# Performance work log

Measured on AMD Instinct MI355X. Metric: run time of the kernel, lower is better.

## Reference

```python
import jax, jax.numpy as jnp
import numpy as np

N = 1024   # num nodes
D = 128    # feat_dim (input_dim)


def setup_inputs() -> dict:
    key = jax.random.key(0)
    k1, k2 = jax.random.split(key)
    x = jax.random.normal(k1, (N, D), dtype=jnp.float32)
    # nn.Linear(D, 1) -> weight vector [D], bias [1] (xavier init weight, zero bias)
    w_vec = jax.random.normal(k2, (D,), dtype=jnp.float32) * np.sqrt(2.0 / (D + 1))
    w_bias = jnp.zeros((1,), dtype=jnp.float32)
    return {"x": x, "w_vec": w_vec, "w_bias": w_bias}


def reference(x, w_vec, w_bias):
    # diff[i, j, d] = |x[i, d] - x[j, d]|  (repeat_interleave row-major -> x[i] minus broadcast x[j])
    diff = jnp.abs(x[:, None, :] - x[None, :, :])          # [N, N, D]
    scores = jnp.einsum('ijd,d->ij', diff, w_vec) + w_bias[0]  # Linear(D,1) -> [N, N]
    scores = jax.nn.relu(scores)
    return jax.nn.softmax(scores, axis=1)
```

## Files before the change

### kernel.cpp

```cpp
#include <hip/hip_runtime.h>

#define N 1024
#define D 128
#define PAD 132

__global__ __launch_bounds__(512, 4) void scores_kernel(
    const float* __restrict__ x, const float* __restrict__ w,
    const float* __restrict__ bias, float* __restrict__ E,
    float* __restrict__ part) {
  __shared__ float sxi[64 * PAD];
  __shared__ float sxj[32 * PAD];
  __shared__ float sw[D];

  const int t  = threadIdx.x;
  const int bi = blockIdx.y * 64;
  const int bj = blockIdx.x * 32;

  {
    const int c  = t & 31;
    const int r0 = t >> 5;
    #pragma unroll
    for (int p = 0; p < 4; ++p) {
      const int r = r0 + p * 16;
      const float4 v = reinterpret_cast<const float4*>(x)[(bi + r) * 32 + c];
      *reinterpret_cast<float4*>(&sxi[r * PAD + c * 4]) = v;
    }
    #pragma unroll
    for (int p = 0; p < 2; ++p) {
      const int r = r0 + p * 16;
      const float4 v = reinterpret_cast<const float4*>(x)[(bj + r) * 32 + c];
      *reinterpret_cast<float4*>(&sxj[r * PAD + c * 4]) = v;
    }
    if (t < 32)
      *reinterpret_cast<float4*>(&sw[t * 4]) =
          reinterpret_cast<const float4*>(w)[t];
  }
  __syncthreads();

  const int g  = __builtin_amdgcn_readfirstlane(t >> 8);
  const int s  = t & 255;
  const int tx = s & 15;
  const int ty = s >> 4;
  const int d0 = g * 64;

  float acc[4][2];
  #pragma unroll
  for (int a = 0; a < 4; ++a)
    #pragma unroll
    for (int b = 0; b < 2; ++b) acc[a][b] = 0.f;

  #pragma unroll 4
  for (int dc = 0; dc < 16; ++dc) {
    const int d = d0 + dc * 4;
    const float4 W = *reinterpret_cast<const float4*>(&sw[d]);
    float4 A[4], B[2];
    #pragma unroll
    for (int a = 0; a < 4; ++a)
      A[a] = *reinterpret_cast<const float4*>(&sxi[(ty + 16 * a) * PAD + d]);
    #pragma unroll
    for (int b = 0; b < 2; ++b)
      B[b] = *reinterpret_cast<const float4*>(&sxj[(tx + 16 * b) * PAD + d]);

    #pragma unroll
    for (int a = 0; a < 4; ++a) {
      #pragma unroll
      for (int b = 0; b < 2; ++b) {
        float v = acc[a][b];
        v = fmaf(fabsf(A[a].x - B[b].x), W.x, v);
        v = fmaf(fabsf(A[a].y - B[b].y), W.y, v);
        v = fmaf(fabsf(A[a].z - B[b].z), W.z, v);
        v = fmaf(fabsf(A[a].w - B[b].w), W.w, v);
        acc[a][b] = v;
      }
    }
  }
  __syncthreads();

  float* comb = sxi;
  if (g == 1) {
    float* dst = comb + s * 9;
    #pragma unroll
    for (int k = 0; k < 8; ++k) dst[k] = acc[k >> 1][k & 1];
  }
  __syncthreads();

  if (g == 0) {
    const float* src = comb + s * 9;
    #pragma unroll
    for (int k = 0; k < 8; ++k) acc[k >> 1][k & 1] += src[k];

    const float bv = bias[0];
    #pragma unroll
    for (int a = 0; a < 4; ++a) {
      float p = 0.f;
      #pragma unroll
      for (int b = 0; b < 2; ++b) {
        const float ev = __expf(fmaxf(acc[a][b] + bv, 0.f));
        acc[a][b] = ev;
        p += ev;
      }
      #pragma unroll
      for (int o = 1; o < 16; o <<= 1) p += __shfl_xor(p, o, 64);
      if (tx == 0) part[(bi + ty + 16 * a) * 32 + blockIdx.x] = p;
    }

    #pragma unroll
    for (int a = 0; a < 4; ++a) {
      const int row = bi + ty + 16 * a;
      #pragma unroll
      for (int b = 0; b < 2; ++b)
        E[row * N + bj + tx + 16 * b] = acc[a][b];
    }
  }
}

__global__ __launch_bounds__(256) void scale_kernel(
    float* __restrict__ S, const float* __restrict__ part) {
  const int row = blockIdx.x;
  const int t   = threadIdx.x;

  float p = part[row * 32 + (t & 31)];
  #pragma unroll
  for (int o = 1; o < 32; o <<= 1) p += __shfl_xor(p, o, 64);
  const float r = 1.0f / p;

  float4* rowp = reinterpret_cast<float4*>(S + row * N);
  float4 v = rowp[t];
  v.x *= r; v.y *= r; v.z *= r; v.w *= r;
  rowp[t] = v;
}

extern "C" void kernel_launch(void* const* d_in, const int* in_sizes, int n_in,
                              void* d_out, int out_size, void* d_ws, size_t ws_size,
                              hipStream_t stream) {
  const float* x = (const float*)d_in[0];
  const float* w = (const float*)d_in[1];
  const float* b = (const float*)d_in[2];
  float* out  = (float*)d_out;
  float* part = (float*)d_ws;

  dim3 grid(N / 32, N / 64);
  scores_kernel<<<grid, 512, 0, stream>>>(x, w, b, out, part);
  scale_kernel<<<N, 256, 0, stream>>>(out, part);
}
```

Measured before the change: 72.83 us.

## Exploit score matrix symmetry by computing only upper-triangle tiles

The pairwise score matrix is symmetric, so the kernel now computes only tiles with block-row index p <= block-column q, decoding each triangle tile index with a sqrt plus correction loop. For off-diagonal tiles it transposes the exponentiated values through shared memory and writes the mirrored tile, emitting separate row-sum partials for the direct and mirrored parts. The scale kernel combines both partial arrays per row. Block size shrinks to 128 threads with a 16x32 tile and the split-D reduction is removed. This roughly halves the abs-diff FMA work at the cost of extra transposed stores, a shared-memory sync and more, smaller blocks.

```diff
diff --git a/kernel.cpp b/kernel.cpp
--- a/kernel.cpp
+++ b/kernel.cpp
@@ -4,32 +4,40 @@
 #define D 128
 #define PAD 132
 
-__global__ __launch_bounds__(512, 4) void scores_kernel(
+__global__ __launch_bounds__(128, 2) void scores_kernel(
     const float* __restrict__ x, const float* __restrict__ w,
     const float* __restrict__ bias, float* __restrict__ E,
-    float* __restrict__ part) {
-  __shared__ float sxi[64 * PAD];
+    float* __restrict__ partA, float* __restrict__ partB) {
+  __shared__ float sxi[16 * PAD];
   __shared__ float sxj[32 * PAD];
   __shared__ float sw[D];
+  __shared__ float ldst[16 * 33];
 
-  const int t  = threadIdx.x;
-  const int bi = blockIdx.y * 64;
-  const int bj = blockIdx.x * 32;
+  const int t = threadIdx.x;
+
+  const int tt = blockIdx.x >> 1;
+  const int h  = blockIdx.x & 1;
+  int q = (int)((sqrtf(8.0f * (float)tt + 1.0f) - 1.0f) * 0.5f);
+  while ((q + 1) * (q + 2) / 2 <= tt) ++q;
+  while (q * (q + 1) / 2 > tt) --q;
+  const int p  = tt - q * (q + 1) / 2;
+  const int bi = p * 32 + h * 16;
+  const int bj = q * 32;
 
   {
     const int c  = t & 31;
     const int r0 = t >> 5;
     #pragma unroll
-    for (int p = 0; p < 4; ++p) {
-      const int r = r0 + p * 16;
-      const float4 v = reinterpret_cast<const float4*>(x)[(bi + r) * 32 + c];
-      *reinterpret_cast<float4*>(&sxi[r * PAD + c * 4]) = v;
+    for (int k = 0; k < 4; ++k) {
+      const int r = r0 + k * 4;
+      *reinterpret_cast<float4*>(&sxi[r * PAD + c * 4]) =
+          reinterpret_cast<const float4*>(x)[(bi + r) * 32 + c];
     }
     #pragma unroll
-    for (int p = 0; p < 2; ++p) {
-      const int r = r0 + p * 16;
-      const float4 v = reinterpret_cast<const float4*>(x)[(bj + r) * 32 + c];
-      *reinterpret_cast<float4*>(&sxj[r * PAD + c * 4]) = v;
+    for (int k = 0; k < 8; ++k) {
+      const int r = r0 + k * 4;
+      *reinterpret_cast<float4*>(&sxj[r * PAD + c * 4]) =
+          reinterpret_cast<const float4*>(x)[(bj + r) * 32 + c];
     }
     if (t < 32)
       *reinterpret_cast<float4*>(&sw[t * 4]) =
@@ -37,32 +45,26 @@
   }
   __syncthreads();
 
-  const int g  = __builtin_amdgcn_readfirstlane(t >> 8);
-  const int s  = t & 255;
-  const int tx = s & 15;
-  const int ty = s >> 4;
-  const int d0 = g * 64;
+  const int tx = t & 15;
+  const int ty = t >> 4;
 
-  float acc[4][2];
-  #pragma unroll
-  for (int a = 0; a < 4; ++a)
-    #pragma unroll
-    for (int b = 0; b < 2; ++b) acc[a][b] = 0.f;
+  float acc[2][2];
+  acc[0][0] = acc[0][1] = acc[1][0] = acc[1][1] = 0.f;
 
   #pragma unroll 4
-  for (int dc = 0; dc < 16; ++dc) {
-    const int d = d0 + dc * 4;
+  for (int dc = 0; dc < 32; ++dc) {
+    const int d = dc * 4;
     const float4 W = *reinterpret_cast<const float4*>(&sw[d]);
-    float4 A[4], B[2];
+    float4 A[2], B[2];
     #pragma unroll
-    for (int a = 0; a < 4; ++a)
-      A[a] = *reinterpret_cast<const float4*>(&sxi[(ty + 16 * a) * PAD + d]);
+    for (int a = 0; a < 2; ++a)
+      A[a] = *reinterpret_cast<const float4*>(&sxi[(ty + 8 * a) * PAD + d]);
     #pragma unroll
     for (int b = 0; b < 2; ++b)
       B[b] = *reinterpret_cast<const float4*>(&sxj[(tx + 16 * b) * PAD + d]);
 
     #pragma unroll
-    for (int a = 0; a < 4; ++a) {
+    for (int a = 0; a < 2; ++a) {
       #pragma unroll
       for (int b = 0; b < 2; ++b) {
         float v = acc[a][b];
@@ -74,60 +76,73 @@
       }
     }
   }
-  __syncthreads();
 
-  float* comb = sxi;
-  if (g == 1) {
-    float* dst = comb + s * 9;
+  const float bv = bias[0];
+  float e[2][2];
+  #pragma unroll
+  for (int a = 0; a < 2; ++a) {
+    float pd = 0.f;
     #pragma unroll
-    for (int k = 0; k < 8; ++k) dst[k] = acc[k >> 1][k & 1];
+    for (int b = 0; b < 2; ++b) {
+      const float ev = __expf(fmaxf(acc[a][b] + bv, 0.f));
+      e[a][b] = ev;
+      pd += ev;
+    }
+    #pragma unroll
+    for (int o = 1; o < 16; o <<= 1) pd += __shfl_xor(pd, o, 64);
+    if (tx == 0) partA[(bi + ty + 8 * a) * 32 + q] = pd;
   }
-  __syncthreads();
 
-  if (g == 0) {
-    const float* src = comb + s * 9;
+  #pragma unroll
+  for (int a = 0; a < 2; ++a) {
+    const int row = bi + ty + 8 * a;
     #pragma unroll
-    for (int k = 0; k < 8; ++k) acc[k >> 1][k & 1] += src[k];
+    for (int b = 0; b < 2; ++b)
+      E[row * N + bj + tx + 16 * b] = e[a][b];
+  }
 
-    const float bv = bias[0];
+  if (p != q) {
     #pragma unroll
-    for (int a = 0; a < 4; ++a) {
-      float p = 0.f;
-      #pragma unroll
-      for (int b = 0; b < 2; ++b) {
-        const float ev = __expf(fmaxf(acc[a][b] + bv, 0.f));
-        acc[a][b] = ev;
-        p += ev;
-      }
-      #pragma unroll
-      for (int o = 1; o < 16; o <<= 1) p += __shfl_xor(p, o, 64);
-      if (tx == 0) part[(bi + ty + 16 * a) * 32 + blockIdx.x] = p;
-    }
-
-    #pragma unroll
-    for (int a = 0; a < 4; ++a) {
-      const int row = bi + ty + 16 * a;
+    for (int a = 0; a < 2; ++a)
       #pragma unroll
       for (int b = 0; b < 2; ++b)
-        E[row * N + bj + tx + 16 * b] = acc[a][b];
-    }
+        ldst[(ty + 8 * a) * 33 + tx + 16 * b] = e[a][b];
+    __syncthreads();
+
+    const int rj = t >> 2;
+    const int c0 = (t & 3) * 4;
+    float v0 = ldst[(c0 + 0) * 33 + rj];
+    float v1 = ldst[(c0 + 1) * 33 + rj];
+    float v2 = ldst[(c0 + 2) * 33 + rj];
+    float v3 = ldst[(c0 + 3) * 33 + rj];
+    *reinterpret_cast<float4*>(&E[(bj + rj) * N + bi + c0]) =
+        make_float4(v0, v1, v2, v3);
+    float ps = (v0 + v1) + (v2 + v3);
+    ps += __shfl_xor(ps, 1, 64);
+    ps += __shfl_xor(ps, 2, 64);
+    if ((t & 3) == 0) partB[(bj + rj) * 64 + 2 * p + h] = ps;
   }
 }
 
 __global__ __launch_bounds__(256) void scale_kernel(
-    float* __restrict__ S, const float* __restrict__ part) {
+    float* __restrict__ S, const float* __restrict__ partA,
+    const float* __restrict__ partB) {
   const int row = blockIdx.x;
+  const int s   = row >> 5;
   const int t   = threadIdx.x;
+  const int l   = t & 63;
 
-  float p = part[row * 32 + (t & 31)];
+  float v = 0.f;
+  if (l < 32 && l >= s) v += partA[row * 32 + l];
+  if (l < 2 * s)        v += partB[row * 64 + l];
   #pragma unroll
-  for (int o = 1; o < 32; o <<= 1) p += __shfl_xor(p, o, 64);
-  const float r = 1.0f / p;
+  for (int o = 1; o < 64; o <<= 1) v += __shfl_xor(v, o, 64);
+  const float r = 1.0f / v;
 
   float4* rowp = reinterpret_cast<float4*>(S + row * N);
-  float4 v = rowp[t];
-  v.x *= r; v.y *= r; v.z *= r; v.w *= r;
-  rowp[t] = v;
+  float4 u = rowp[t];
+  u.x *= r; u.y *= r; u.z *= r; u.w *= r;
+  rowp[t] = u;
 }
 
 extern "C" void kernel_launch(void* const* d_in, const int* in_sizes, int n_in,
@@ -136,10 +151,10 @@
   const float* x = (const float*)d_in[0];
   const float* w = (const float*)d_in[1];
   const float* b = (const float*)d_in[2];
-  float* out  = (float*)d_out;
-  float* part = (float*)d_ws;
+  float* out = (float*)d_out;
+  float* partA = (float*)d_ws;
+  float* partB = partA + 1024 * 32;
 
-  dim3 grid(N / 32, N / 64);
-  scores_kernel<<<grid, 512, 0, stream>>>(x, w, b, out, part);
-  scale_kernel<<<N, 256, 0, stream>>>(out, part);
+  scores_kernel<<<1056, 128, 0, stream>>>(x, w, b, out, partA, partB);
+  scale_kernel<<<N, 256, 0, stream>>>(out, partA, partB);
 }
```

Measured after the change: 71.05 us. -2.4%, faster.
